# Performance work log

Measured on AMD Instinct MI355X. Metric: run time of the kernel, lower is better.

## Reference

```python
import jax, jax.numpy as jnp
import numpy as np

GAMMA = 1.0  # gamma=1.0, train_gamma=False -> constant


def setup_inputs() -> dict:
    key = jax.random.key(0)
    k1, k2, k3, k4 = jax.random.split(key, 4)
    B, T, d_in, d_state, d_out = 32, 4096, 128, 128, 128
    u = jax.random.normal(k1, (B, T, d_in), dtype=jnp.float32)
    x0 = jax.random.normal(k2, (B, d_state), dtype=jnp.float32)
    S = 0.1 * jax.random.normal(k3, (d_state, d_state), dtype=jnp.float32)
    K_raw = jax.random.normal(k4, (d_state + d_out, d_state + d_in), dtype=jnp.float32)
    return {"u": u, "x0": x0, "S": S, "K_raw": K_raw}


def _ssm_matrices(S, K_raw):
    d_x = S.shape[0]
    # contraction: K = K_raw / (sigma + 0.002), sigma = ||K_raw||_2 clamped at 1e-5
    sigma = jnp.maximum(jnp.linalg.norm(K_raw, ord=2), 1e-5)
    K = K_raw / (sigma + 0.002)
    K11 = K[:d_x, :d_x]
    K12 = K[:d_x, d_x:]
    K21 = K[d_x:, :d_x]
    K22 = K[d_x:, d_x:]
    Sinv = jnp.linalg.inv(S)
    A = Sinv @ K11 @ S
    Bm = GAMMA * (Sinv @ K12)
    C = K21 @ S
    D = GAMMA * K22
    return A, Bm, C, D


def reference(u, x0, S, K_raw):
    # u: (B, T, d_in); x0: (B, d_state)
    A, Bm, C, D = _ssm_matrices(S, K_raw)
    At, Bt, Ct, Dt = A.T, Bm.T, C.T, D.T
    uT = jnp.transpose(u, (1, 0, 2))  # (T, B, d_in)

    def step(x, u_t):
        y_t = x @ Ct + u_t @ Dt          # (B, d_out)
        x_next = x @ At + u_t @ Bt       # (B, d_state)
        return x_next, (x, y_t)

    _, (xs, ys) = jax.lax.scan(step, x0, uT)
    y_seq = jnp.transpose(ys, (1, 0, 2))  # (B, T, d_out)
    x_seq = jnp.transpose(xs, (1, 0, 2))  # (B, T, d_state)
    return (y_seq, x_seq)
```

## Files before the change

kernel.cpp:

```cpp
#include <hip/hip_runtime.h>


#define B_   32
#define T_   4096
#define D_   128
#define LCH  16
#define NCH  256

#define O_MSQ0    0LL
#define O_MSQ1    65536LL
#define O_PART    131072LL
#define O_Z0      131200LL
#define O_Z1      147584LL
#define O_TN      163968LL
#define O_WA      180352LL
#define O_WB      196736LL
#define O_WC      213120LL
#define O_WD      229504LL
#define O_SINVT   245888LL
#define O_V0      262272LL
#define O_PW      266368LL
#define O_CONTRIB 397440LL
#define O_SC      1446016LL
#define O_SSUP    1511552LL
#define O_SCHUNK  1577088LL
#define WS_FLOATS 2625664LL

__global__ void k_m0(const float* __restrict__ N, float* __restrict__ M0, float* __restrict__ part) {
  __shared__ float TA[32][36], TB[32][36], dbuf[32];
  const int t  = threadIdx.x;
  const int ab = blockIdx.x >> 3, bb = blockIdx.x & 7;
  const int a0 = ab * 32, b0 = bb * 32;
  const int ar = t >> 3, c4 = (t & 7) << 2;
  float s0 = 0.f, s1 = 0.f, s2 = 0.f, s3 = 0.f;
  for (int r0 = 0; r0 < 256; r0 += 32) {
    const int rr = t >> 3, cc = (t & 7) << 2;
    *(float4*)&TA[rr][cc] = *(const float4*)&N[(r0 + rr) * 256 + a0 + cc];
    *(float4*)&TB[rr][cc] = *(const float4*)&N[(r0 + rr) * 256 + b0 + cc];
    __syncthreads();
#pragma unroll 8
    for (int r = 0; r < 32; r++) {
      const float av = TA[r][ar];
      const float4 bv = *(const float4*)&TB[r][c4];
      s0 += av * bv.x; s1 += av * bv.y; s2 += av * bv.z; s3 += av * bv.w;
    }
    __syncthreads();
  }
  float4 o; o.x = s0; o.y = s1; o.z = s2; o.w = s3;
  *(float4*)&M0[(a0 + ar) * 256 + b0 + c4] = o;
  if (ab == bb) {
    const int d = ar - c4;
    if (d >= 0 && d < 4) dbuf[ar] = (d == 0) ? s0 : (d == 1) ? s1 : (d == 2) ? s2 : s3;
    __syncthreads();
    if (t == 0) { float s = 0.f; for (int i = 0; i < 32; i++) s += dbuf[i]; part[ab] = s; }
  }
}

__global__ void k_sq(const float* __restrict__ X, float* __restrict__ Y,
                     const float* __restrict__ pIn, float* __restrict__ pOut) {
  __shared__ float TA[32][36], TB[32][36], dbuf[32];
  float c = 0.f;
#pragma unroll
  for (int i = 0; i < 8; i++) c += pIn[i];
  const float ic2 = 1.0f / (c * c);
  const int t  = threadIdx.x;
  const int ab = blockIdx.x >> 3, bb = blockIdx.x & 7;
  const int a0 = ab * 32, b0 = bb * 32;
  const int ar = t >> 3, c4 = (t & 7) << 2;
  float s0 = 0.f, s1 = 0.f, s2 = 0.f, s3 = 0.f;
  for (int m0 = 0; m0 < 256; m0 += 32) {
    const int rr = t >> 3, cc = (t & 7) << 2;
    *(float4*)&TA[rr][cc] = *(const float4*)&X[(a0 + rr) * 256 + m0 + cc];
    *(float4*)&TB[rr][cc] = *(const float4*)&X[(m0 + rr) * 256 + b0 + cc];
    __syncthreads();
#pragma unroll 8
    for (int m = 0; m < 32; m++) {
      const float av = TA[ar][m];
      const float4 bv = *(const float4*)&TB[m][c4];
      s0 += av * bv.x; s1 += av * bv.y; s2 += av * bv.z; s3 += av * bv.w;
    }
    __syncthreads();
  }
  s0 *= ic2; s1 *= ic2; s2 *= ic2; s3 *= ic2;
  float4 o; o.x = s0; o.y = s1; o.z = s2; o.w = s3;
  *(float4*)&Y[(a0 + ar) * 256 + b0 + c4] = o;
  if (ab == bb) {
    const int d = ar - c4;
    if (d >= 0 && d < 4) dbuf[ar] = (d == 0) ? s0 : (d == 1) ? s1 : (d == 2) ? s2 : s3;
    __syncthreads();
    if (t == 0) { float s = 0.f; for (int i = 0; i < 32; i++) s += dbuf[i]; pOut[ab] = s; }
  }
}

__global__ __launch_bounds__(256, 1) void k_gj(const float* __restrict__ S, float* __restrict__ Z) {
  __shared__ float LCol[128];
  const int c = threadIdx.x;
  float4 a4[32];
  if (c < 128) {
#pragma unroll
    for (int q = 0; q < 32; q++) {
      a4[q].x = S[(4 * q + 0) * 128 + c]; a4[q].y = S[(4 * q + 1) * 128 + c];
      a4[q].z = S[(4 * q + 2) * 128 + c]; a4[q].w = S[(4 * q + 3) * 128 + c];
    }
  } else {
    const int d = c - 128;
#pragma unroll
    for (int q = 0; q < 32; q++) {
      a4[q].x = (d == 4 * q + 0) ? 1.f : 0.f; a4[q].y = (d == 4 * q + 1) ? 1.f : 0.f;
      a4[q].z = (d == 4 * q + 2) ? 1.f : 0.f; a4[q].w = (d == 4 * q + 3) ? 1.f : 0.f;
    }
  }
  for (int p = 0; p < 128; p++) {
    if (c == p) {
#pragma unroll
      for (int q = 0; q < 32; q++) *(float4*)&LCol[4 * q] = a4[q];
    }
    __syncthreads();
    float4 sq = a4[0];
#pragma unroll
    for (int q = 1; q < 32; q++) if ((p >> 2) == q) sq = a4[q];
    const int pm = p & 3;
    const float ap = pm == 0 ? sq.x : pm == 1 ? sq.y : pm == 2 ? sq.z : sq.w;
    const float aps = ap / LCol[p];
#pragma unroll
    for (int q = 0; q < 32; q++) {
      const float4 L = *(const float4*)&LCol[4 * q];
      float4 v = a4[q];
      v.x = (4 * q + 0 == p) ? aps : v.x - L.x * aps;
      v.y = (4 * q + 1 == p) ? aps : v.y - L.y * aps;
      v.z = (4 * q + 2 == p) ? aps : v.z - L.z * aps;
      v.w = (4 * q + 3 == p) ? aps : v.w - L.w * aps;
      a4[q] = v;
    }
    __syncthreads();
  }
  if (c >= 128) {
    const int cc = c - 128;
#pragma unroll
    for (int q = 0; q < 32; q++) {
      Z[(4 * q + 0) * 128 + cc] = a4[q].x; Z[(4 * q + 1) * 128 + cc] = a4[q].y;
      Z[(4 * q + 2) * 128 + cc] = a4[q].z; Z[(4 * q + 3) * 128 + cc] = a4[q].w;
    }
  }
}

__global__ void k_mm(const float* __restrict__ A, const float* __restrict__ Bm,
                     float* __restrict__ Dst, const float* __restrict__ C, int mode) {
  __shared__ float TA[32][36], TB[32][36];
  const int t  = threadIdx.x;
  const int ab = blockIdx.x >> 2, bb = blockIdx.x & 3;
  const int a0 = ab * 32, b0 = bb * 32;
  const int ar = t >> 3, c4 = (t & 7) << 2;
  float s0 = 0.f, s1 = 0.f, s2 = 0.f, s3 = 0.f;
  for (int m0 = 0; m0 < 128; m0 += 32) {
    const int rr = t >> 3, cc = (t & 7) << 2;
    *(float4*)&TA[rr][cc] = *(const float4*)&A[(a0 + rr) * 128 + m0 + cc];
    *(float4*)&TB[rr][cc] = *(const float4*)&Bm[(m0 + rr) * 128 + b0 + cc];
    __syncthreads();
#pragma unroll 8
    for (int m = 0; m < 32; m++) {
      const float av = TA[ar][m];
      const float4 bv = *(const float4*)&TB[m][c4];
      s0 += av * bv.x; s1 += av * bv.y; s2 += av * bv.z; s3 += av * bv.w;
    }
    __syncthreads();
  }
  const int oi = (a0 + ar) * 128 + b0 + c4;
  if (mode == 1) {
    s0 = 2.f * C[oi + 0] - s0; s1 = 2.f * C[oi + 1] - s1;
    s2 = 2.f * C[oi + 2] - s2; s3 = 2.f * C[oi + 3] - s3;
  }
  float4 o; o.x = s0; o.y = s1; o.z = s2; o.w = s3;
  *(float4*)&Dst[oi] = o;
}

__global__ void k_ops(const float* __restrict__ Kraw, const float* __restrict__ S,
                      const float* __restrict__ x0, const float* __restrict__ part,
                      const float* __restrict__ Z, float* __restrict__ WA, float* __restrict__ WB,
                      float* __restrict__ WC, float* __restrict__ WD,
                      float* __restrict__ SinvT, float* __restrict__ v0) {
  double logl = 0.0, w = 1.0;
  for (int k = 0; k <= 10; k++) {
    double c = 0.0;
    for (int i = 0; i < 8; i++) c += (double)part[k * 8 + i];
    logl += w * log2(c); w *= 0.5;
  }
  double sigma = exp2(0.5 * logl);
  if (sigma < 1e-5) sigma = 1e-5;
  const float invs = (float)(1.0 / (sigma + 0.002));
  const int wg = blockIdx.x, t = threadIdx.x;
  if (wg < 4) {
    float* dst = wg == 0 ? WA : wg == 1 ? WB : wg == 2 ? WC : WD;
    const int ro = (wg >> 1) * 128, co = (wg & 1) * 128;
    for (int e = t; e < 16384; e += 256) {
      const int i = e >> 7, o = e & 127;
      dst[e] = Kraw[(ro + o) * 256 + co + i] * invs;
    }
  } else if (wg == 4) {
    for (int e = t; e < 16384; e += 256) {
      const int i = e >> 7, o = e & 127;
      SinvT[e] = Z[o * 128 + i];
    }
  } else {
    for (int e = t; e < 4096; e += 256) {
      const int b = e >> 7, o = e & 127;
      float s = 0.f;
      for (int i = 0; i < 128; i++) s += x0[b * 128 + i] * S[o * 128 + i];
      v0[e] = s;
    }
  }
}

template <int MODE>
__global__ __launch_bounds__(512) void k_scan(const float* __restrict__ u,
                                              const float* __restrict__ WAg,
                                              const float* __restrict__ WBg,
                                              const float* __restrict__ initp,
                                              float* __restrict__ outv,
                                              float* __restrict__ contribp) {
  extern __shared__ float lds[];
  float* WAl  = lds;
  float* WBuf = lds + 16384;
  float* XU   = lds + 24576;
  const int t   = threadIdx.x;
  const int w   = blockIdx.x;
  const int gr0 = w * 32;
  const int b   = gr0 >> 8;
  const int c0  = gr0 & 255;
  for (int e = t * 4; e < 16384; e += 2048)
    *(float4*)&WAl[e] = *(const float4*)&WAg[e];
  for (int e = t * 4; e < 4096; e += 2048) {
    const int r = e >> 7, i = e & 127;
    if (MODE == 1) {
      const float4 a = *(const float4*)&initp[((gr0 + r) << 7) + i];
      XU[(i + 0) * 36 + r] = a.x; XU[(i + 1) * 36 + r] = a.y;
      XU[(i + 2) * 36 + r] = a.z; XU[(i + 3) * 36 + r] = a.w;
    } else {
      XU[(i + 0) * 36 + r] = 0.f; XU[(i + 1) * 36 + r] = 0.f;
      XU[(i + 2) * 36 + r] = 0.f; XU[(i + 3) * 36 + r] = 0.f;
    }
  }
  __syncthreads();
  const int rt = t >> 5, ot = t & 31;
  const int r0 = rt * 2, o0 = ot * 4;
  for (int j = 0; j < LCH; j++) {
    for (int e = t * 4; e < 4096; e += 2048) {
      const int r = e >> 7, i = e & 127;
      const int gidx = (((b << 12) + (c0 + r) * LCH + j) << 7) + i;
      if (MODE == 1) {
        float4 a;
        a.x = XU[(i + 0) * 36 + r]; a.y = XU[(i + 1) * 36 + r];
        a.z = XU[(i + 2) * 36 + r]; a.w = XU[(i + 3) * 36 + r];
        *(float4*)&outv[gidx] = a;
      }
      const float4 uv = *(const float4*)&u[gidx];
      XU[(128 + i + 0) * 36 + r] = uv.x; XU[(128 + i + 1) * 36 + r] = uv.y;
      XU[(128 + i + 2) * 36 + r] = uv.z; XU[(128 + i + 3) * 36 + r] = uv.w;
    }
    __syncthreads();
    float4 acc0, acc1;
    acc0.x = acc0.y = acc0.z = acc0.w = 0.f;
    acc1.x = acc1.y = acc1.z = acc1.w = 0.f;
#pragma unroll 4
    for (int i = 0; i < 128; i++) {
      const float2 xv = *(const float2*)&XU[i * 36 + r0];
      const float4 wv = *(const float4*)&WAl[(i << 7) + o0];
      acc0.x += xv.x * wv.x; acc0.y += xv.x * wv.y; acc0.z += xv.x * wv.z; acc0.w += xv.x * wv.w;
      acc1.x += xv.y * wv.x; acc1.y += xv.y * wv.y; acc1.z += xv.y * wv.z; acc1.w += xv.y * wv.w;
    }
    for (int half = 0; half < 2; half++) {
      for (int e = t * 4; e < 8192; e += 2048)
        *(float4*)&WBuf[e] = *(const float4*)&WBg[half * 8192 + e];
      __syncthreads();
      const int ibase = 128 + half * 64;
#pragma unroll 4
      for (int i = 0; i < 64; i++) {
        const float2 xv = *(const float2*)&XU[(ibase + i) * 36 + r0];
        const float4 wv = *(const float4*)&WBuf[(i << 7) + o0];
        acc0.x += xv.x * wv.x; acc0.y += xv.x * wv.y; acc0.z += xv.x * wv.z; acc0.w += xv.x * wv.w;
        acc1.x += xv.y * wv.x; acc1.y += xv.y * wv.y; acc1.z += xv.y * wv.z; acc1.w += xv.y * wv.w;
      }
      if (half == 0) __syncthreads();
    }
    XU[(o0 + 0) * 36 + r0 + 0] = acc0.x; XU[(o0 + 1) * 36 + r0 + 0] = acc0.y;
    XU[(o0 + 2) * 36 + r0 + 0] = acc0.z; XU[(o0 + 3) * 36 + r0 + 0] = acc0.w;
    XU[(o0 + 0) * 36 + r0 + 1] = acc1.x; XU[(o0 + 1) * 36 + r0 + 1] = acc1.y;
    XU[(o0 + 2) * 36 + r0 + 1] = acc1.z; XU[(o0 + 3) * 36 + r0 + 1] = acc1.w;
    __syncthreads();
  }
  if (MODE == 0) {
    for (int e = t * 4; e < 4096; e += 2048) {
      const int r = e >> 7, i = e & 127;
      float4 a;
      a.x = XU[(i + 0) * 36 + r]; a.y = XU[(i + 1) * 36 + r];
      a.z = XU[(i + 2) * 36 + r]; a.w = XU[(i + 3) * 36 + r];
      *(float4*)&contribp[((gr0 + r) << 7) + i] = a;
    }
  }
}

__global__ void k_comb(const float* __restrict__ P, const float* __restrict__ initv,
                       const float* __restrict__ add, float* __restrict__ st,
                       float* __restrict__ fin, int mode) {
  extern __shared__ float lds[];
  float* Pl = lds;
  float* tc = lds + 16896;
  float* pb = lds + 17024;
  const int blk = blockIdx.x, t = threadIdx.x;
  const int o = t & 127, h = t >> 7;
  int addBase = 0, stBase = 0, iIdx = 0, fIdx = 0;
  if (mode == 0) { const int bb = blk >> 4, gg = blk & 15; addBase = bb * 256 + gg * 16; fIdx = bb * 16 + gg; }
  else if (mode == 1) { const int bb = blk; addBase = bb * 16; stBase = bb * 16; iIdx = bb; }
  else { const int bb = blk >> 4, gg = blk & 15; addBase = bb * 256 + gg * 16; stBase = addBase; iIdx = bb * 16 + gg; }
  for (int e = t * 4; e < 16384; e += 1024) {
    const int i = e >> 7, oo = e & 127;
    *(float4*)&Pl[i * 132 + oo] = *(const float4*)&P[e];
  }
  if (h == 0) tc[o] = (mode == 0) ? 0.f : initv[iIdx * 128 + o];
  __syncthreads();
  for (int k = 0; k < 16; k++) {
    float s = 0.f;
#pragma unroll 8
    for (int i = 0; i < 64; i++) {
      const int ii = h * 64 + i;
      s += tc[ii] * Pl[ii * 132 + o];
    }
    pb[h * 128 + o] = s;
    __syncthreads();
    if (h == 0) {
      if (mode != 0) st[(stBase + k) * 128 + o] = tc[o];
      tc[o] = pb[o] + pb[128 + o] + add[(addBase + k) * 128 + o];
    }
    __syncthreads();
  }
  if (mode == 0 && h == 0) fin[fIdx * 128 + o] = tc[o];
}

__global__ __launch_bounds__(512) void k_phy(const float* __restrict__ v, const float* __restrict__ u,
                                             const float* __restrict__ WCg, const float* __restrict__ WDg,
                                             float* __restrict__ y) {
  extern __shared__ float lds[];
  float* Wl = lds;
  float* VT = lds + 16896;
  const int t = threadIdx.x;
  const int m0 = blockIdx.x * 64;
  const int rt = t >> 4, ot = t & 15;
  const int r0 = rt * 2, o0 = ot * 8;
  float4 a0l, a0h, a1l, a1h;
  a0l.x = a0l.y = a0l.z = a0l.w = 0.f; a0h = a0l; a1l = a0l; a1h = a0l;
  for (int pass = 0; pass < 2; pass++) {
    const float* W = pass ? WDg : WCg;
    const float* A = pass ? u : v;
    for (int e = t * 4; e < 16384; e += 2048) {
      const int i = e >> 7, oo = e & 127;
      *(float4*)&Wl[i * 132 + oo] = *(const float4*)&W[e];
    }
    for (int e = t * 4; e < 8192; e += 2048) {
      const int r = e >> 7, i = e & 127;
      const float4 a = *(const float4*)&A[((m0 + r) << 7) + i];
      VT[(i + 0) * 68 + r] = a.x; VT[(i + 1) * 68 + r] = a.y;
      VT[(i + 2) * 68 + r] = a.z; VT[(i + 3) * 68 + r] = a.w;
    }
    __syncthreads();
#pragma unroll 2
    for (int i = 0; i < 128; i++) {
      const float2 xv = *(const float2*)&VT[i * 68 + r0];
      const float4 w0 = *(const float4*)&Wl[i * 132 + o0];
      const float4 w1 = *(const float4*)&Wl[i * 132 + o0 + 4];
      a0l.x += xv.x * w0.x; a0l.y += xv.x * w0.y; a0l.z += xv.x * w0.z; a0l.w += xv.x * w0.w;
      a0h.x += xv.x * w1.x; a0h.y += xv.x * w1.y; a0h.z += xv.x * w1.z; a0h.w += xv.x * w1.w;
      a1l.x += xv.y * w0.x; a1l.y += xv.y * w0.y; a1l.z += xv.y * w0.z; a1l.w += xv.y * w0.w;
      a1h.x += xv.y * w1.x; a1h.y += xv.y * w1.y; a1h.z += xv.y * w1.z; a1h.w += xv.y * w1.w;
    }
    __syncthreads();
  }
  *(float4*)&y[((m0 + r0 + 0) << 7) + o0] = a0l;
  *(float4*)&y[((m0 + r0 + 0) << 7) + o0 + 4] = a0h;
  *(float4*)&y[((m0 + r0 + 1) << 7) + o0] = a1l;
  *(float4*)&y[((m0 + r0 + 1) << 7) + o0 + 4] = a1h;
}

__global__ __launch_bounds__(512) void k_phx(float* __restrict__ vx, const float* __restrict__ Wg) {
  extern __shared__ float lds[];
  float* Wl = lds;
  float* VT = lds + 16896;
  const int t = threadIdx.x;
  const int m0 = blockIdx.x * 64;
  const int rt = t >> 4, ot = t & 15;
  const int r0 = rt * 2, o0 = ot * 8;
  float4 a0l, a0h, a1l, a1h;
  a0l.x = a0l.y = a0l.z = a0l.w = 0.f; a0h = a0l; a1l = a0l; a1h = a0l;
  for (int e = t * 4; e < 16384; e += 2048) {
    const int i = e >> 7, oo = e & 127;
    *(float4*)&Wl[i * 132 + oo] = *(const float4*)&Wg[e];
  }
  for (int e = t * 4; e < 8192; e += 2048) {
    const int r = e >> 7, i = e & 127;
    const float4 a = *(const float4*)&vx[((m0 + r) << 7) + i];
    VT[(i + 0) * 68 + r] = a.x; VT[(i + 1) * 68 + r] = a.y;
    VT[(i + 2) * 68 + r] = a.z; VT[(i + 3) * 68 + r] = a.w;
  }
  __syncthreads();
#pragma unroll 2
  for (int i = 0; i < 128; i++) {
    const float2 xv = *(const float2*)&VT[i * 68 + r0];
    const float4 w0 = *(const float4*)&Wl[i * 132 + o0];
    const float4 w1 = *(const float4*)&Wl[i * 132 + o0 + 4];
    a0l.x += xv.x * w0.x; a0l.y += xv.x * w0.y; a0l.z += xv.x * w0.z; a0l.w += xv.x * w0.w;
    a0h.x += xv.x * w1.x; a0h.y += xv.x * w1.y; a0h.z += xv.x * w1.z; a0h.w += xv.x * w1.w;
    a1l.x += xv.y * w0.x; a1l.y += xv.y * w0.y; a1l.z += xv.y * w0.z; a1l.w += xv.y * w0.w;
    a1h.x += xv.y * w1.x; a1h.y += xv.y * w1.y; a1h.z += xv.y * w1.z; a1h.w += xv.y * w1.w;
  }
  *(float4*)&vx[((m0 + r0 + 0) << 7) + o0] = a0l;
  *(float4*)&vx[((m0 + r0 + 0) << 7) + o0 + 4] = a0h;
  *(float4*)&vx[((m0 + r0 + 1) << 7) + o0] = a1l;
  *(float4*)&vx[((m0 + r0 + 1) << 7) + o0 + 4] = a1h;
}

extern "C" void kernel_launch(void* const* d_in, const int* in_sizes, int n_in,
                              void* d_out, int out_size, void* d_ws, size_t ws_size,
                              hipStream_t stream) {
  (void)in_sizes; (void)n_in; (void)out_size;
  const float* u    = (const float*)d_in[0];
  const float* x0   = (const float*)d_in[1];
  const float* S    = (const float*)d_in[2];
  const float* Kraw = (const float*)d_in[3];
  float* out = (float*)d_out;
  float* yout = out;
  float* vx   = out + 16777216LL;
  float* ws = (float*)d_ws;
  if (ws_size < (size_t)(WS_FLOATS * 4)) return;

  float* MSQ0 = ws + O_MSQ0;  float* MSQ1 = ws + O_MSQ1;  float* PART = ws + O_PART;
  float* Z0 = ws + O_Z0;      float* Z1 = ws + O_Z1;      float* TN = ws + O_TN;
  float* WA = ws + O_WA;      float* WB = ws + O_WB;      float* WC = ws + O_WC;
  float* WD = ws + O_WD;      float* SINVT = ws + O_SINVT; float* V0 = ws + O_V0;
  float* PW = ws + O_PW;
  float* CONTRIB = ws + O_CONTRIB;  float* SC = ws + O_SC;
  float* SSUP = ws + O_SSUP;        float* SCHUNK = ws + O_SCHUNK;

  k_m0<<<64, 256, 0, stream>>>(Kraw, MSQ0, PART);
  float* mb[2] = {MSQ0, MSQ1};
  for (int k = 1; k <= 10; k++)
    k_sq<<<64, 256, 0, stream>>>(mb[(k + 1) & 1], mb[k & 1], PART + (k - 1) * 8, PART + k * 8);

  k_gj<<<1, 256, 0, stream>>>(S, Z0);
  k_mm<<<16, 256, 0, stream>>>(S, Z0, TN, nullptr, 0);
  k_mm<<<16, 256, 0, stream>>>(Z0, TN, Z1, Z0, 1);
  k_mm<<<16, 256, 0, stream>>>(S, Z1, TN, nullptr, 0);
  k_mm<<<16, 256, 0, stream>>>(Z1, TN, Z0, Z1, 1);
  k_mm<<<16, 256, 0, stream>>>(S, Z0, TN, nullptr, 0);
  k_mm<<<16, 256, 0, stream>>>(Z0, TN, Z1, Z0, 1);

  k_ops<<<6, 256, 0, stream>>>(Kraw, S, x0, PART, Z1, WA, WB, WC, WD, SINVT, V0);

  k_mm<<<16, 256, 0, stream>>>(WA, WA, PW + 0, nullptr, 0);
  k_mm<<<16, 256, 0, stream>>>(PW + 0, PW + 0, PW + 16384, nullptr, 0);
  k_mm<<<16, 256, 0, stream>>>(PW + 16384, PW + 16384, PW + 32768, nullptr, 0);
  k_mm<<<16, 256, 0, stream>>>(PW + 32768, PW + 32768, PW + 49152, nullptr, 0);
  k_mm<<<16, 256, 0, stream>>>(PW + 49152, PW + 49152, PW + 65536, nullptr, 0);
  k_mm<<<16, 256, 0, stream>>>(PW + 65536, PW + 65536, PW + 81920, nullptr, 0);
  k_mm<<<16, 256, 0, stream>>>(PW + 81920, PW + 81920, PW + 98304, nullptr, 0);
  k_mm<<<16, 256, 0, stream>>>(PW + 98304, PW + 98304, PW + 114688, nullptr, 0);
  float* P16 = PW + 49152;
  float* P256 = PW + 114688;

  const size_t scanLds = 135168;
  const size_t combLds = 69120;
  const size_t gemmLds = 102400;

  k_scan<0><<<256, 512, scanLds, stream>>>(u, WA, WB, nullptr, nullptr, CONTRIB);
  k_comb<<<512, 256, combLds, stream>>>(P16, nullptr, CONTRIB, nullptr, SC, 0);
  k_comb<<<32, 256, combLds, stream>>>(P256, V0, SC, SSUP, nullptr, 1);
  k_comb<<<512, 256, combLds, stream>>>(P16, SSUP, CONTRIB, SCHUNK, nullptr, 2);
  k_scan<1><<<256, 512, scanLds, stream>>>(u, WA, WB, SCHUNK, vx, nullptr);
  k_phy<<<2048, 512, gemmLds, stream>>>(vx, u, WC, WD, yout);
  k_phx<<<2048, 512, gemmLds, stream>>>(vx, SINVT);
}
```

Before: 1.426 ms.

## Fold preprocessing kernel chain into two persistent kernels with grid barriers

```diff
diff --git a/kernel.cpp b/kernel.cpp
--- a/kernel.cpp
+++ b/kernel.cpp
@@ -6,6 +6,7 @@
 #define D_   128
 #define LCH  16
 #define NCH  256
+#define NSIG 10
 
 #define O_MSQ0    0LL
 #define O_MSQ1    65536LL
@@ -26,141 +27,36 @@
 #define O_SCHUNK  1577088LL
 #define WS_FLOATS 2625664LL
 
-__global__ void k_m0(const float* __restrict__ N, float* __restrict__ M0, float* __restrict__ part) {
-  __shared__ float TA[32][36], TB[32][36], dbuf[32];
+__device__ __forceinline__ void gbar(int* cnt, int n) {
+  __syncthreads();
+  if (threadIdx.x == 0) {
+    __threadfence();
+    atomicAdd(cnt, 1);
+    while (atomicAdd(cnt, 0) < n) { }
+    __threadfence();
+  }
+  __syncthreads();
+  __threadfence();
+}
+
+__device__ void mult32(const float* __restrict__ A, const float* __restrict__ Bm,
+                       float* __restrict__ Dst, const float* __restrict__ C,
+                       int mode, int wl) {
+  __shared__ float MTA[32][36], MTB[32][36];
   const int t  = threadIdx.x;
-  const int ab = blockIdx.x >> 3, bb = blockIdx.x & 7;
-  const int a0 = ab * 32, b0 = bb * 32;
-  const int ar = t >> 3, c4 = (t & 7) << 2;
-  float s0 = 0.f, s1 = 0.f, s2 = 0.f, s3 = 0.f;
-  for (int r0 = 0; r0 < 256; r0 += 32) {
-    const int rr = t >> 3, cc = (t & 7) << 2;
-    *(float4*)&TA[rr][cc] = *(const float4*)&N[(r0 + rr) * 256 + a0 + cc];
-    *(float4*)&TB[rr][cc] = *(const float4*)&N[(r0 + rr) * 256 + b0 + cc];
-    __syncthreads();
-#pragma unroll 8
-    for (int r = 0; r < 32; r++) {
-      const float av = TA[r][ar];
-      const float4 bv = *(const float4*)&TB[r][c4];
-      s0 += av * bv.x; s1 += av * bv.y; s2 += av * bv.z; s3 += av * bv.w;
-    }
-    __syncthreads();
-  }
-  float4 o; o.x = s0; o.y = s1; o.z = s2; o.w = s3;
-  *(float4*)&M0[(a0 + ar) * 256 + b0 + c4] = o;
-  if (ab == bb) {
-    const int d = ar - c4;
-    if (d >= 0 && d < 4) dbuf[ar] = (d == 0) ? s0 : (d == 1) ? s1 : (d == 2) ? s2 : s3;
-    __syncthreads();
-    if (t == 0) { float s = 0.f; for (int i = 0; i < 32; i++) s += dbuf[i]; part[ab] = s; }
-  }
-}
-
-__global__ void k_sq(const float* __restrict__ X, float* __restrict__ Y,
-                     const float* __restrict__ pIn, float* __restrict__ pOut) {
-  __shared__ float TA[32][36], TB[32][36], dbuf[32];
-  float c = 0.f;
-#pragma unroll
-  for (int i = 0; i < 8; i++) c += pIn[i];
-  const float ic2 = 1.0f / (c * c);
-  const int t  = threadIdx.x;
-  const int ab = blockIdx.x >> 3, bb = blockIdx.x & 7;
-  const int a0 = ab * 32, b0 = bb * 32;
-  const int ar = t >> 3, c4 = (t & 7) << 2;
-  float s0 = 0.f, s1 = 0.f, s2 = 0.f, s3 = 0.f;
-  for (int m0 = 0; m0 < 256; m0 += 32) {
-    const int rr = t >> 3, cc = (t & 7) << 2;
-    *(float4*)&TA[rr][cc] = *(const float4*)&X[(a0 + rr) * 256 + m0 + cc];
-    *(float4*)&TB[rr][cc] = *(const float4*)&X[(m0 + rr) * 256 + b0 + cc];
-    __syncthreads();
-#pragma unroll 8
-    for (int m = 0; m < 32; m++) {
-      const float av = TA[ar][m];
-      const float4 bv = *(const float4*)&TB[m][c4];
-      s0 += av * bv.x; s1 += av * bv.y; s2 += av * bv.z; s3 += av * bv.w;
-    }
-    __syncthreads();
-  }
-  s0 *= ic2; s1 *= ic2; s2 *= ic2; s3 *= ic2;
-  float4 o; o.x = s0; o.y = s1; o.z = s2; o.w = s3;
-  *(float4*)&Y[(a0 + ar) * 256 + b0 + c4] = o;
-  if (ab == bb) {
-    const int d = ar - c4;
-    if (d >= 0 && d < 4) dbuf[ar] = (d == 0) ? s0 : (d == 1) ? s1 : (d == 2) ? s2 : s3;
-    __syncthreads();
-    if (t == 0) { float s = 0.f; for (int i = 0; i < 32; i++) s += dbuf[i]; pOut[ab] = s; }
-  }
-}
-
-__global__ __launch_bounds__(256, 1) void k_gj(const float* __restrict__ S, float* __restrict__ Z) {
-  __shared__ float LCol[128];
-  const int c = threadIdx.x;
-  float4 a4[32];
-  if (c < 128) {
-#pragma unroll
-    for (int q = 0; q < 32; q++) {
-      a4[q].x = S[(4 * q + 0) * 128 + c]; a4[q].y = S[(4 * q + 1) * 128 + c];
-      a4[q].z = S[(4 * q + 2) * 128 + c]; a4[q].w = S[(4 * q + 3) * 128 + c];
-    }
-  } else {
-    const int d = c - 128;
-#pragma unroll
-    for (int q = 0; q < 32; q++) {
-      a4[q].x = (d == 4 * q + 0) ? 1.f : 0.f; a4[q].y = (d == 4 * q + 1) ? 1.f : 0.f;
-      a4[q].z = (d == 4 * q + 2) ? 1.f : 0.f; a4[q].w = (d == 4 * q + 3) ? 1.f : 0.f;
-    }
-  }
-  for (int p = 0; p < 128; p++) {
-    if (c == p) {
-#pragma unroll
-      for (int q = 0; q < 32; q++) *(float4*)&LCol[4 * q] = a4[q];
-    }
-    __syncthreads();
-    float4 sq = a4[0];
-#pragma unroll
-    for (int q = 1; q < 32; q++) if ((p >> 2) == q) sq = a4[q];
-    const int pm = p & 3;
-    const float ap = pm == 0 ? sq.x : pm == 1 ? sq.y : pm == 2 ? sq.z : sq.w;
-    const float aps = ap / LCol[p];
-#pragma unroll
-    for (int q = 0; q < 32; q++) {
-      const float4 L = *(const float4*)&LCol[4 * q];
-      float4 v = a4[q];
-      v.x = (4 * q + 0 == p) ? aps : v.x - L.x * aps;
-      v.y = (4 * q + 1 == p) ? aps : v.y - L.y * aps;
-      v.z = (4 * q + 2 == p) ? aps : v.z - L.z * aps;
-      v.w = (4 * q + 3 == p) ? aps : v.w - L.w * aps;
-      a4[q] = v;
-    }
-    __syncthreads();
-  }
-  if (c >= 128) {
-    const int cc = c - 128;
-#pragma unroll
-    for (int q = 0; q < 32; q++) {
-      Z[(4 * q + 0) * 128 + cc] = a4[q].x; Z[(4 * q + 1) * 128 + cc] = a4[q].y;
-      Z[(4 * q + 2) * 128 + cc] = a4[q].z; Z[(4 * q + 3) * 128 + cc] = a4[q].w;
-    }
-  }
-}
-
-__global__ void k_mm(const float* __restrict__ A, const float* __restrict__ Bm,
-                     float* __restrict__ Dst, const float* __restrict__ C, int mode) {
-  __shared__ float TA[32][36], TB[32][36];
-  const int t  = threadIdx.x;
-  const int ab = blockIdx.x >> 2, bb = blockIdx.x & 3;
+  const int ab = wl >> 2, bb = wl & 3;
   const int a0 = ab * 32, b0 = bb * 32;
   const int ar = t >> 3, c4 = (t & 7) << 2;
   float s0 = 0.f, s1 = 0.f, s2 = 0.f, s3 = 0.f;
   for (int m0 = 0; m0 < 128; m0 += 32) {
     const int rr = t >> 3, cc = (t & 7) << 2;
-    *(float4*)&TA[rr][cc] = *(const float4*)&A[(a0 + rr) * 128 + m0 + cc];
-    *(float4*)&TB[rr][cc] = *(const float4*)&Bm[(m0 + rr) * 128 + b0 + cc];
+    *(float4*)&MTA[rr][cc] = *(const float4*)&A[(a0 + rr) * 128 + m0 + cc];
+    *(float4*)&MTB[rr][cc] = *(const float4*)&Bm[(m0 + rr) * 128 + b0 + cc];
     __syncthreads();
 #pragma unroll 8
     for (int m = 0; m < 32; m++) {
-      const float av = TA[ar][m];
-      const float4 bv = *(const float4*)&TB[m][c4];
+      const float av = MTA[ar][m];
+      const float4 bv = *(const float4*)&MTB[m][c4];
       s0 += av * bv.x; s1 += av * bv.y; s2 += av * bv.z; s3 += av * bv.w;
     }
     __syncthreads();
@@ -174,39 +70,182 @@
   *(float4*)&Dst[oi] = o;
 }
 
-__global__ void k_ops(const float* __restrict__ Kraw, const float* __restrict__ S,
-                      const float* __restrict__ x0, const float* __restrict__ part,
-                      const float* __restrict__ Z, float* __restrict__ WA, float* __restrict__ WB,
-                      float* __restrict__ WC, float* __restrict__ WD,
-                      float* __restrict__ SinvT, float* __restrict__ v0) {
-  double logl = 0.0, w = 1.0;
-  for (int k = 0; k <= 10; k++) {
-    double c = 0.0;
-    for (int i = 0; i < 8; i++) c += (double)part[k * 8 + i];
-    logl += w * log2(c); w *= 0.5;
-  }
-  double sigma = exp2(0.5 * logl);
-  if (sigma < 1e-5) sigma = 1e-5;
-  const float invs = (float)(1.0 / (sigma + 0.002));
+__global__ __launch_bounds__(256, 1) void k_prep1(
+    const float* __restrict__ Kraw, const float* __restrict__ S,
+    const float* __restrict__ x0,
+    float* __restrict__ MSQ0, float* __restrict__ MSQ1, float* __restrict__ PART,
+    float* __restrict__ Z0, float* __restrict__ WA, float* __restrict__ WB,
+    float* __restrict__ WC, float* __restrict__ WD, float* __restrict__ V0,
+    int* __restrict__ BAR) {
   const int wg = blockIdx.x, t = threadIdx.x;
-  if (wg < 4) {
-    float* dst = wg == 0 ? WA : wg == 1 ? WB : wg == 2 ? WC : WD;
-    const int ro = (wg >> 1) * 128, co = (wg & 1) * 128;
-    for (int e = t; e < 16384; e += 256) {
-      const int i = e >> 7, o = e & 127;
-      dst[e] = Kraw[(ro + o) * 256 + co + i] * invs;
-    }
-  } else if (wg == 4) {
-    for (int e = t; e < 16384; e += 256) {
-      const int i = e >> 7, o = e & 127;
-      SinvT[e] = Z[o * 128 + i];
-    }
+
+  if (wg == 64) {
+    __shared__ float LCol[128];
+    const int c = t;
+    float4 a4[32];
+    if (c < 128) {
+#pragma unroll
+      for (int q = 0; q < 32; q++) {
+        a4[q].x = S[(4 * q + 0) * 128 + c]; a4[q].y = S[(4 * q + 1) * 128 + c];
+        a4[q].z = S[(4 * q + 2) * 128 + c]; a4[q].w = S[(4 * q + 3) * 128 + c];
+      }
+    } else {
+      const int d = c - 128;
+#pragma unroll
+      for (int q = 0; q < 32; q++) {
+        a4[q].x = (d == 4 * q + 0) ? 1.f : 0.f; a4[q].y = (d == 4 * q + 1) ? 1.f : 0.f;
+        a4[q].z = (d == 4 * q + 2) ? 1.f : 0.f; a4[q].w = (d == 4 * q + 3) ? 1.f : 0.f;
+      }
+    }
+    for (int p = 0; p < 128; p++) {
+      if (c == p) {
+#pragma unroll
+        for (int q = 0; q < 32; q++) *(float4*)&LCol[4 * q] = a4[q];
+      }
+      __syncthreads();
+      float4 sq = a4[0];
+#pragma unroll
+      for (int q = 1; q < 32; q++) if ((p >> 2) == q) sq = a4[q];
+      const int pm = p & 3;
+      const float ap = pm == 0 ? sq.x : pm == 1 ? sq.y : pm == 2 ? sq.z : sq.w;
+      const float aps = ap / LCol[p];
+#pragma unroll
+      for (int q = 0; q < 32; q++) {
+        const float4 L = *(const float4*)&LCol[4 * q];
+        float4 v = a4[q];
+        v.x = (4 * q + 0 == p) ? aps : v.x - L.x * aps;
+        v.y = (4 * q + 1 == p) ? aps : v.y - L.y * aps;
+        v.z = (4 * q + 2 == p) ? aps : v.z - L.z * aps;
+        v.w = (4 * q + 3 == p) ? aps : v.w - L.w * aps;
+        a4[q] = v;
+      }
+      __syncthreads();
+    }
+    if (c >= 128) {
+      const int cc = c - 128;
+#pragma unroll
+      for (int q = 0; q < 32; q++) {
+        Z0[(4 * q + 0) * 128 + cc] = a4[q].x; Z0[(4 * q + 1) * 128 + cc] = a4[q].y;
+        Z0[(4 * q + 2) * 128 + cc] = a4[q].z; Z0[(4 * q + 3) * 128 + cc] = a4[q].w;
+      }
+    }
+    return;
+  }
+
+  __shared__ float TA[32][36], TB[32][36], dbuf[32];
+  const int ab = wg >> 3, bb = wg & 7;
+  const int a0 = ab * 32, b0 = bb * 32;
+  const int ar = t >> 3, c4 = (t & 7) << 2;
+
+  {
+    float s0 = 0.f, s1 = 0.f, s2 = 0.f, s3 = 0.f;
+    for (int r0 = 0; r0 < 256; r0 += 32) {
+      const int rr = t >> 3, cc = (t & 7) << 2;
+      *(float4*)&TA[rr][cc] = *(const float4*)&Kraw[(r0 + rr) * 256 + a0 + cc];
+      *(float4*)&TB[rr][cc] = *(const float4*)&Kraw[(r0 + rr) * 256 + b0 + cc];
+      __syncthreads();
+#pragma unroll 8
+      for (int r = 0; r < 32; r++) {
+        const float av = TA[r][ar];
+        const float4 bv = *(const float4*)&TB[r][c4];
+        s0 += av * bv.x; s1 += av * bv.y; s2 += av * bv.z; s3 += av * bv.w;
+      }
+      __syncthreads();
+    }
+    float4 o; o.x = s0; o.y = s1; o.z = s2; o.w = s3;
+    *(float4*)&MSQ0[(a0 + ar) * 256 + b0 + c4] = o;
+    if (ab == bb) {
+      const int d = ar - c4;
+      if (d >= 0 && d < 4) dbuf[ar] = (d == 0) ? s0 : (d == 1) ? s1 : (d == 2) ? s2 : s3;
+      __syncthreads();
+      if (t == 0) { float s = 0.f; for (int i = 0; i < 32; i++) s += dbuf[i]; PART[ab] = s; }
+    }
+  }
+  gbar(BAR + 0, 64);
+
+  float* bufs[2] = {MSQ0, MSQ1};
+  for (int k = 1; k <= NSIG; k++) {
+    const float* X = bufs[(k + 1) & 1];
+    float* Y = bufs[k & 1];
+    float c = 0.f;
+#pragma unroll
+    for (int i = 0; i < 8; i++) c += PART[(k - 1) * 8 + i];
+    const float ic2 = 1.0f / (c * c);
+    float s0 = 0.f, s1 = 0.f, s2 = 0.f, s3 = 0.f;
+    for (int m0 = 0; m0 < 256; m0 += 32) {
+      const int rr = t >> 3, cc = (t & 7) << 2;
+      *(float4*)&TA[rr][cc] = *(const float4*)&X[(a0 + rr) * 256 + m0 + cc];
+      *(float4*)&TB[rr][cc] = *(const float4*)&X[(m0 + rr) * 256 + b0 + cc];
+      __syncthreads();
+#pragma unroll 8
+      for (int m = 0; m < 32; m++) {
+        const float av = TA[ar][m];
+        const float4 bv = *(const float4*)&TB[m][c4];
+        s0 += av * bv.x; s1 += av * bv.y; s2 += av * bv.z; s3 += av * bv.w;
+      }
+      __syncthreads();
+    }
+    s0 *= ic2; s1 *= ic2; s2 *= ic2; s3 *= ic2;
+    float4 o; o.x = s0; o.y = s1; o.z = s2; o.w = s3;
+    *(float4*)&Y[(a0 + ar) * 256 + b0 + c4] = o;
+    if (ab == bb) {
+      const int d = ar - c4;
+      if (d >= 0 && d < 4) dbuf[ar] = (d == 0) ? s0 : (d == 1) ? s1 : (d == 2) ? s2 : s3;
+      __syncthreads();
+      if (t == 0) { float s = 0.f; for (int i = 0; i < 32; i++) s += dbuf[i]; PART[k * 8 + ab] = s; }
+    }
+    gbar(BAR + k, 64);
+  }
+
+  if (wg < 5) {
+    double logl = 0.0, w = 1.0;
+    for (int k = 0; k <= NSIG; k++) {
+      double c = 0.0;
+      for (int i = 0; i < 8; i++) c += (double)PART[k * 8 + i];
+      logl += w * log2(c); w *= 0.5;
+    }
+    double sigma = exp2(0.5 * logl);
+    if (sigma < 1e-5) sigma = 1e-5;
+    const float invs = (float)(1.0 / (sigma + 0.002));
+    if (wg < 4) {
+      float* dst = wg == 0 ? WA : wg == 1 ? WB : wg == 2 ? WC : WD;
+      const int ro = (wg >> 1) * 128, co = (wg & 1) * 128;
+      for (int e = t; e < 16384; e += 256) {
+        const int i = e >> 7, o = e & 127;
+        dst[e] = Kraw[(ro + o) * 256 + co + i] * invs;
+      }
+    } else {
+      for (int e = t; e < 4096; e += 256) {
+        const int b = e >> 7, o = e & 127;
+        float s = 0.f;
+        for (int i = 0; i < 128; i++) s += x0[b * 128 + i] * S[o * 128 + i];
+        V0[e] = s;
+      }
+    }
+  }
+}
+
+__global__ __launch_bounds__(256, 1) void k_prep2(
+    const float* __restrict__ S, float* __restrict__ Z0, float* __restrict__ Z1,
+    float* __restrict__ TN, const float* __restrict__ WA, float* __restrict__ PW,
+    float* __restrict__ SINVT, int* __restrict__ BARA, int* __restrict__ BARB) {
+  const int wg = blockIdx.x, t = threadIdx.x;
+  if (wg < 16) {
+    mult32(S, Z0, TN, nullptr, 0, wg);  gbar(BARA + 0, 16);
+    mult32(Z0, TN, Z1, Z0, 1, wg);      gbar(BARA + 1, 16);
+    mult32(S, Z1, TN, nullptr, 0, wg);  gbar(BARA + 2, 16);
+    mult32(Z1, TN, Z0, Z1, 1, wg);      gbar(BARA + 3, 16);
+    mult32(S, Z0, TN, nullptr, 0, wg);  gbar(BARA + 4, 16);
+    mult32(Z0, TN, Z1, Z0, 1, wg);      gbar(BARA + 5, 16);
+    for (int e = wg * 256 + t; e < 16384; e += 4096)
+      SINVT[e] = Z1[(e & 127) * 128 + (e >> 7)];
   } else {
-    for (int e = t; e < 4096; e += 256) {
-      const int b = e >> 7, o = e & 127;
-      float s = 0.f;
-      for (int i = 0; i < 128; i++) s += x0[b * 128 + i] * S[o * 128 + i];
-      v0[e] = s;
+    const int wl = wg - 16;
+    mult32(WA, WA, PW, nullptr, 0, wl);                          gbar(BARB + 0, 16);
+#pragma unroll 1
+    for (int q = 1; q < 8; q++) {
+      mult32(PW + (q - 1) * 16384, PW + (q - 1) * 16384, PW + q * 16384, nullptr, 0, wl);
+      if (q < 7) gbar(BARB + q, 16);
     }
   }
 }
@@ -438,30 +477,14 @@
   float* PW = ws + O_PW;
   float* CONTRIB = ws + O_CONTRIB;  float* SC = ws + O_SC;
   float* SSUP = ws + O_SSUP;        float* SCHUNK = ws + O_SCHUNK;
-
-  k_m0<<<64, 256, 0, stream>>>(Kraw, MSQ0, PART);
-  float* mb[2] = {MSQ0, MSQ1};
-  for (int k = 1; k <= 10; k++)
-    k_sq<<<64, 256, 0, stream>>>(mb[(k + 1) & 1], mb[k & 1], PART + (k - 1) * 8, PART + k * 8);
-
-  k_gj<<<1, 256, 0, stream>>>(S, Z0);
-  k_mm<<<16, 256, 0, stream>>>(S, Z0, TN, nullptr, 0);
-  k_mm<<<16, 256, 0, stream>>>(Z0, TN, Z1, Z0, 1);
-  k_mm<<<16, 256, 0, stream>>>(S, Z1, TN, nullptr, 0);
-  k_mm<<<16, 256, 0, stream>>>(Z1, TN, Z0, Z1, 1);
-  k_mm<<<16, 256, 0, stream>>>(S, Z0, TN, nullptr, 0);
-  k_mm<<<16, 256, 0, stream>>>(Z0, TN, Z1, Z0, 1);
-
-  k_ops<<<6, 256, 0, stream>>>(Kraw, S, x0, PART, Z1, WA, WB, WC, WD, SINVT, V0);
-
-  k_mm<<<16, 256, 0, stream>>>(WA, WA, PW + 0, nullptr, 0);
-  k_mm<<<16, 256, 0, stream>>>(PW + 0, PW + 0, PW + 16384, nullptr, 0);
-  k_mm<<<16, 256, 0, stream>>>(PW + 16384, PW + 16384, PW + 32768, nullptr, 0);
-  k_mm<<<16, 256, 0, stream>>>(PW + 32768, PW + 32768, PW + 49152, nullptr, 0);
-  k_mm<<<16, 256, 0, stream>>>(PW + 49152, PW + 49152, PW + 65536, nullptr, 0);
-  k_mm<<<16, 256, 0, stream>>>(PW + 65536, PW + 65536, PW + 81920, nullptr, 0);
-  k_mm<<<16, 256, 0, stream>>>(PW + 81920, PW + 81920, PW + 98304, nullptr, 0);
-  k_mm<<<16, 256, 0, stream>>>(PW + 98304, PW + 98304, PW + 114688, nullptr, 0);
+  int* BAR = (int*)(ws + O_PART + 96);
+
+  hipMemsetAsync((void*)BAR, 0, 32 * sizeof(int), stream);
+
+  k_prep1<<<65, 256, 0, stream>>>(Kraw, S, x0, MSQ0, MSQ1, PART, Z0,
+                                  WA, WB, WC, WD, V0, BAR);
+  k_prep2<<<32, 256, 0, stream>>>(S, Z0, Z1, TN, WA, PW, SINVT, BAR + 16, BAR + 24);
+
   float* P16 = PW + 49152;
   float* P256 = PW + 114688;
 
```

Result: faster. 1.234 ms (-13.5%).
